# Kernel tuning notes

Measured on AMD Instinct MI355X. Metric: run time of the kernel, lower is better.

Reference implementation:

```python
import jax, jax.numpy as jnp
import numpy as np

D_MODEL, D_K, D_V, H, M = 1024, 64, 64, 16, 40


def setup_inputs() -> dict:
    key = jax.random.key(0)
    ks = jax.random.split(key, 16)
    b, nq, nk = 8, 1024, 1024
    inp = {
        "queries": jax.random.normal(ks[0], (b, nq, D_MODEL), jnp.float32),
        "keys": jax.random.normal(ks[1], (b, nk, D_MODEL), jnp.float32),
        "values": jax.random.normal(ks[2], (b, nk, D_MODEL), jnp.float32),
        "attention_mask": jax.random.randint(ks[3], (b, H, nq, nk), 0, 2) > 0,
        # Linear params, parametrized as x @ W + b (W has shape (in, out)).
        "Wq": jax.random.normal(ks[4], (D_MODEL, H * D_K), jnp.float32) * 0.03,
        "bq": jnp.zeros((H * D_K,), jnp.float32),
        "Wk": jax.random.normal(ks[5], (D_MODEL, H * D_K), jnp.float32) * 0.03,
        "bk": jnp.zeros((H * D_K,), jnp.float32),
        "Wv": jax.random.normal(ks[6], (D_MODEL, H * D_V), jnp.float32) * 0.03,
        "bv": jnp.zeros((H * D_V,), jnp.float32),
        "Wo": jax.random.normal(ks[7], (H * D_V, D_MODEL), jnp.float32) * 0.03,
        "bo": jnp.zeros((D_MODEL,), jnp.float32),
        # Memory slots: m_k ~ N(0, 1/d_k), m_v ~ N(0, 1/m), shape (1, m, h*d)
        "m_k": jax.random.normal(ks[8], (1, M, H * D_K), jnp.float32) / D_K,
        "m_v": jax.random.normal(ks[9], (1, M, H * D_V), jnp.float32) / M,
    }
    return inp


def reference(queries, keys, values, attention_mask, Wq, bq, Wk, bk, Wv, bv, Wo, bo, m_k, m_v):
    b, nq, _ = queries.shape
    nk = keys.shape[1]
    scale = jnp.asarray(np.sqrt(D_K), jnp.float32)

    # scaled memory slots, broadcast over batch
    mk = scale * jnp.broadcast_to(m_k, (b, M, H * D_K))
    mv = jnp.asarray(np.sqrt(M), jnp.float32) * jnp.broadcast_to(m_v, (b, M, H * D_V))

    q = (queries @ Wq + bq).reshape(b, nq, H, D_K).transpose(0, 2, 1, 3)       # b h nq dk
    k = jnp.concatenate([keys @ Wk + bk, mk], axis=1)                           # b (nk+m) h*dk
    k = k.reshape(b, nk + M, H, D_K).transpose(0, 2, 1, 3)                      # b h (nk+m) dk
    v = jnp.concatenate([values @ Wv + bv, mv], axis=1)
    v = v.reshape(b, nk + M, H, D_V).transpose(0, 2, 1, 3)                      # b h (nk+m) dv

    att = jnp.einsum('bhqd,bhkd->bhqk', q, k) / scale                           # b h nq (nk+m)
    # mask only real keys; memory slots always attendable
    att_real = jnp.where(attention_mask, -jnp.inf, att[:, :, :, :nk])
    att = jnp.concatenate([att_real, att[:, :, :, nk:]], axis=-1)
    att = jax.nn.softmax(att, axis=-1)

    out = jnp.einsum('bhqk,bhkd->bhqd', att, v)
    out = out.transpose(0, 2, 1, 3).reshape(b, nq, H * D_V)
    out = out @ Wo + bo
    return out, att
```

## Files before the change

kernel.cpp:

```cpp
#include <hip/hip_runtime.h>
#include <hip/hip_bf16.h>


#define B_ 8
#define NQ 1024
#define NK 1024
#define DM 1024
#define H_ 16
#define DK 64
#define NKM 1064
#define NKP 1104
#define PSTR 280

typedef __attribute__((ext_vector_type(8))) short bf16x8;
typedef __attribute__((ext_vector_type(4))) float f32x4;
typedef __attribute__((ext_vector_type(4))) short short4v;

static __device__ __forceinline__ short f2bf(float x) {
    __hip_bfloat16 h = __float2bfloat16(x);
    return __builtin_bit_cast(short, h);
}
static __device__ __forceinline__ float bf2f(short s) {
    unsigned int u = ((unsigned int)(unsigned short)s) << 16;
    return __builtin_bit_cast(float, u);
}

static __device__ __forceinline__ bf16x8 pack8(const float* __restrict__ p) {
    float4 f0 = *(const float4*)p;
    float4 f1 = *(const float4*)(p + 4);
    bf16x8 a;
    a[0] = f2bf(f0.x); a[1] = f2bf(f0.y); a[2] = f2bf(f0.z); a[3] = f2bf(f0.w);
    a[4] = f2bf(f1.x); a[5] = f2bf(f1.y); a[6] = f2bf(f1.z); a[7] = f2bf(f1.w);
    return a;
}

static __device__ __forceinline__ void gload16(const short* g, short* l) {
    __builtin_amdgcn_global_load_lds(
        (__attribute__((address_space(1))) void*)const_cast<short*>(g),
        (__attribute__((address_space(3))) void*)l, 16, 0, 0);
}

__global__ void detect_mask_kernel(const unsigned int* __restrict__ m, int n_dwords,
                                   int* __restrict__ flag) {
    __shared__ int any_big;
    if (threadIdx.x == 0) any_big = 0;
    __syncthreads();
    for (int i = threadIdx.x; i < n_dwords; i += blockDim.x)
        if (m[i] > 1u) any_big = 1;
    __syncthreads();
    if (threadIdx.x == 0) *flag = any_big ? 0 : 1;
}

__global__ void transpose_w_kernel(const float* __restrict__ W, short* __restrict__ WT) {
    __shared__ float t[32][33];
    int tx = threadIdx.x & 31, ty = threadIdx.x >> 5;
    int k0 = blockIdx.x * 32, n0 = blockIdx.y * 32;
#pragma unroll
    for (int r = 0; r < 4; r++)
        t[ty + 8 * r][tx] = W[(size_t)(k0 + ty + 8 * r) * DM + n0 + tx];
    __syncthreads();
#pragma unroll
    for (int r = 0; r < 4; r++)
        WT[(size_t)(n0 + ty + 8 * r) * DM + k0 + tx] = f2bf(t[tx][ty + 8 * r]);
}

__global__ void convert_bf16_kernel(const float* __restrict__ a, const float* __restrict__ b,
                                    const float* __restrict__ c, short* __restrict__ out) {
    const size_t NT = (size_t)B_ * NQ * DM;
    const size_t total = NT * 3;
    size_t i = ((size_t)blockIdx.x * 256 + threadIdx.x) * 8;
    const size_t step = (size_t)gridDim.x * 256 * 8;
    for (; i < total; i += step) {
        const float* src = (i < NT) ? (a + i) : (i < 2 * NT) ? (b + (i - NT)) : (c + (i - 2 * NT));
        *(bf16x8*)(out + i) = pack8(src);
    }
}

__global__ void fill_mem_kernel(const float* __restrict__ m_k, const float* __restrict__ m_v,
                                short* __restrict__ Kh, short* __restrict__ Vt) {
    int blk = blockIdx.x;
    int bh = blk / 20, rb = blk % 20;
    int r = rb * 4 + (threadIdx.x >> 6);
    int d = threadIdx.x & 63;
    int h = bh & 15;
    float kv = 0.f, vv = 0.f;
    if (r < 40) {
        kv = 8.0f * m_k[(size_t)(r * H_ + h) * DK + d];
        vv = 6.324555320336759f * m_v[(size_t)(r * H_ + h) * DK + d];
    }
    int kk = 1024 + r;
    Kh[((size_t)bh * NKP + kk) * 64 + d] = f2bf(kv);
    Vt[((size_t)bh * 64 + d) * NKP + kk] = f2bf(vv);
}

template <int MODE>
__global__ __launch_bounds__(256) void gemm_tile_kernel(
    const short* __restrict__ Ab, const short* __restrict__ BT,
    const float* __restrict__ bias,
    float* __restrict__ outF, short* __restrict__ outB) {
    __shared__ short As[2][4096];
    __shared__ short Bs[2][4096];

    const int tid = threadIdx.x;
    const int lane = tid & 63;
    const int wid = tid >> 6;
    int swz = (blockIdx.x & 7) * 64 + (blockIdx.x >> 3);
    const int mt = swz >> 3, nt = swz & 7;
    const int brow = mt * 128, bcol = nt * 128;
    const int wr = wid >> 1, wc = wid & 1;
    const int l15 = lane & 15, lg = lane >> 4;

    f32x4 acc[4][4];
#pragma unroll
    for (int m = 0; m < 4; m++)
#pragma unroll
        for (int n = 0; n < 4; n++) acc[m][n] = f32x4{0.f, 0.f, 0.f, 0.f};

    auto stage = [&](int buf, int k0) {
#pragma unroll
        for (int i = 0; i < 2; i++) {
            int c = tid + i * 256;
            int row = c >> 2, slot = c & 3;
            int base = (c & ~63) * 8;
            gload16(Ab + (size_t)(brow + row) * DM + k0 + slot * 8, &As[buf][base]);
            gload16(BT + (size_t)(bcol + row) * DM + k0 + slot * 8, &Bs[buf][base]);
        }
    };

    stage(0, 0);
    for (int kt = 0; kt < 32; ++kt) {
        __syncthreads();
        if (kt + 1 < 32) stage((kt + 1) & 1, (kt + 1) * 32);
        const short* Ab_ = As[kt & 1];
        const short* Bb_ = Bs[kt & 1];
        bf16x8 a[4], b[4];
#pragma unroll
        for (int m = 0; m < 4; m++)
            a[m] = *(const bf16x8*)(Ab_ + (wr * 64 + m * 16 + l15) * 32 + lg * 8);
#pragma unroll
        for (int n = 0; n < 4; n++)
            b[n] = *(const bf16x8*)(Bb_ + (wc * 64 + n * 16 + l15) * 32 + lg * 8);
#pragma unroll
        for (int m = 0; m < 4; m++)
#pragma unroll
            for (int n = 0; n < 4; n++)
                acc[m][n] = __builtin_amdgcn_mfma_f32_16x16x32_bf16(a[m], b[n], acc[m][n], 0, 0, 0);
    }

#pragma unroll
    for (int n = 0; n < 4; n++) {
        int col = bcol + wc * 64 + n * 16 + l15;
        float bval = bias[col];
#pragma unroll
        for (int m = 0; m < 4; m++) {
            int row0 = brow + wr * 64 + m * 16 + lg * 4;
            if (MODE == 3) {
#pragma unroll
                for (int r = 0; r < 4; r++)
                    outF[(size_t)(row0 + r) * DM + col] = acc[m][n][r] + bval;
            } else if (MODE == 0) {
                int h = col >> 6, d = col & 63;
#pragma unroll
                for (int r = 0; r < 4; r++) {
                    int row = row0 + r;
                    int b = row >> 10, q = row & 1023;
                    outB[((size_t)(b * H_ + h) * NQ + q) * 64 + d] = f2bf(acc[m][n][r] + bval);
                }
            } else if (MODE == 1) {
                int h = col >> 6, d = col & 63;
#pragma unroll
                for (int r = 0; r < 4; r++) {
                    int row = row0 + r;
                    int b = row >> 10, kk = row & 1023;
                    outB[((size_t)(b * H_ + h) * NKP + kk) * 64 + d] = f2bf(acc[m][n][r] + bval);
                }
            } else {
                int h = col >> 6, d = col & 63;
                int b = row0 >> 10, kk0 = row0 & 1023;
                short4v sv;
#pragma unroll
                for (int r = 0; r < 4; r++) sv[r] = f2bf(acc[m][n][r] + bval);
                *(short4v*)(outB + ((size_t)(b * H_ + h) * 64 + d) * NKP + kk0) = sv;
            }
        }
    }
}

__global__ __launch_bounds__(256) void attn_fused_kernel(
    const short* __restrict__ Qh, const short* __restrict__ Kh,
    const short* __restrict__ Vt,
    const unsigned char* __restrict__ mb, const int* __restrict__ mi,
    const int* __restrict__ flag,
    float* __restrict__ att, short* __restrict__ Ow) {
    __shared__ short Pl[4][16][PSTR];
    __shared__ float redS[4][16];

    int swz = (blockIdx.x & 7) * 1024 + (blockIdx.x >> 3);
    int bh = swz >> 6;
    int q0 = (swz & 63) * 16;
    int wid = threadIdx.x >> 6;
    int lane = threadIdx.x & 63;
    int l15 = lane & 15, lg = lane >> 4;

    const short* Qb = Qh + (size_t)bh * NQ * 64;
    const short* Kb = Kh + (size_t)bh * NKP * 64;
    const short* Vb = Vt + (size_t)bh * 64 * NKP;
    const int is32 = *flag;

    bf16x8 aq0 = *(const bf16x8*)(Qb + (size_t)(q0 + l15) * 64 + lg * 8);
    bf16x8 aq1 = *(const bf16x8*)(Qb + (size_t)(q0 + l15) * 64 + 32 + lg * 8);

    size_t qrow = (size_t)bh * NQ + q0 + l15;
    const int kkw = wid * 272;

    float rs = 0.f;
    for (int t = 0; t < 17; ++t) {
        int kt = kkw + t * 16;
        const short* Kr = Kb + (size_t)(kt + l15) * 64;
        bf16x8 k0 = *(const bf16x8*)(Kr + lg * 8);
        bf16x8 k1 = *(const bf16x8*)(Kr + 32 + lg * 8);
        f32x4 s = {0.f, 0.f, 0.f, 0.f};
        s = __builtin_amdgcn_mfma_f32_16x16x32_bf16(k0, aq0, s, 0, 0, 0);
        s = __builtin_amdgcn_mfma_f32_16x16x32_bf16(k1, aq1, s, 0, 0, 0);
        int kkbase = kt + lg * 4;
        unsigned mu = 0;
        if (kkbase < NK) {
            if (is32) {
                int4 mv = *(const int4*)(mi + qrow * NK + kkbase);
                mu = (mv.x ? 1u : 0u) | (mv.y ? 0x100u : 0u) |
                     (mv.z ? 0x10000u : 0u) | (mv.w ? 0x1000000u : 0u);
            } else {
                mu = *(const unsigned*)(mb + qrow * NK + kkbase);
            }
        }
        short4v pv;
#pragma unroll
        for (int r = 0; r < 4; r++) {
            bool dead = (kkbase + r >= NKM) || (((mu >> (8 * r)) & 0xffu) != 0u);
            float e = dead ? 0.f : __expf(s[r] * 0.125f);
            rs += e;
            pv[r] = f2bf(e);
        }
        *(short4v*)(&Pl[wid][l15][t * 16 + lg * 4]) = pv;
    }
    rs += __shfl_xor(rs, 16);
    rs += __shfl_xor(rs, 32);
    if (lg == 0) redS[wid][l15] = rs;
    __syncthreads();
    float invq = 1.f / (redS[0][l15] + redS[1][l15] + redS[2][l15] + redS[3][l15]);

    f32x4 po[4];
#pragma unroll
    for (int dt = 0; dt < 4; dt++) po[dt] = f32x4{0.f, 0.f, 0.f, 0.f};

    for (int pp = 0; pp < 9; ++pp) {
        int kks = kkw + pp * 32 + lg * 8;
        bool val = (pp < 8) | (lg < 2);
        bf16x8 a = bf16x8{0, 0, 0, 0, 0, 0, 0, 0};
        if (val) a = *(const bf16x8*)(&Pl[wid][l15][pp * 32 + lg * 8]);
        if (val && kks < NKM) {
            float4 w0, w1;
            w0.x = bf2f(a[0]) * invq; w0.y = bf2f(a[1]) * invq;
            w0.z = bf2f(a[2]) * invq; w0.w = bf2f(a[3]) * invq;
            w1.x = bf2f(a[4]) * invq; w1.y = bf2f(a[5]) * invq;
            w1.z = bf2f(a[6]) * invq; w1.w = bf2f(a[7]) * invq;
            *(float4*)(att + qrow * NKM + kks) = w0;
            *(float4*)(att + qrow * NKM + kks + 4) = w1;
        }
#pragma unroll
        for (int dt = 0; dt < 4; dt++) {
            bf16x8 bv = *(const bf16x8*)(Vb + (size_t)(dt * 16 + l15) * NKP + kkw + pp * 32 + lg * 8);
            po[dt] = __builtin_amdgcn_mfma_f32_16x16x32_bf16(a, bv, po[dt], 0, 0, 0);
        }
    }

    float* OredW = (float*)&Pl[wid][0][0];
#pragma unroll
    for (int dt = 0; dt < 4; dt++)
#pragma unroll
        for (int r = 0; r < 4; r++)
            OredW[(lg * 4 + r) * 68 + dt * 16 + l15] = po[dt][r];
    __syncthreads();

    int tq = threadIdx.x >> 4;
    int d0 = (threadIdx.x & 15) * 4;
    float4 o = {0.f, 0.f, 0.f, 0.f};
#pragma unroll
    for (int w = 0; w < 4; w++) {
        const float* Or = (const float*)&Pl[w][0][0];
        float4 v = *(const float4*)(&Or[tq * 68 + d0]);
        o.x += v.x; o.y += v.y; o.z += v.z; o.w += v.w;
    }
    float invt = 1.f / (redS[0][tq] + redS[1][tq] + redS[2][tq] + redS[3][tq]);
    int b = bh >> 4, h = bh & 15;
    short4v sv;
    sv[0] = f2bf(o.x * invt); sv[1] = f2bf(o.y * invt);
    sv[2] = f2bf(o.z * invt); sv[3] = f2bf(o.w * invt);
    *(short4v*)(Ow + ((size_t)b * NQ + q0 + tq) * DM + h * 64 + d0) = sv;
}

extern "C" void kernel_launch(void* const* d_in, const int* in_sizes, int n_in,
                              void* d_out, int out_size, void* d_ws, size_t ws_size,
                              hipStream_t stream) {
    const float* queries = (const float*)d_in[0];
    const float* keys    = (const float*)d_in[1];
    const float* values  = (const float*)d_in[2];
    const void*  mask    = d_in[3];
    const float* Wq = (const float*)d_in[4];
    const float* bq = (const float*)d_in[5];
    const float* Wk = (const float*)d_in[6];
    const float* bk = (const float*)d_in[7];
    const float* Wv = (const float*)d_in[8];
    const float* bv = (const float*)d_in[9];
    const float* Wo = (const float*)d_in[10];
    const float* bo = (const float*)d_in[11];
    const float* m_k = (const float*)d_in[12];
    const float* m_v = (const float*)d_in[13];

    short* WqT = (short*)d_ws;
    short* WkT = WqT + (size_t)DM * DM;
    short* WvT = WkT + (size_t)DM * DM;
    short* WoT = WvT + (size_t)DM * DM;
    short* Qh  = WoT + (size_t)DM * DM;
    short* Kh  = Qh + (size_t)B_ * H_ * NQ * DK;
    short* Vt  = Kh + (size_t)B_ * H_ * NKP * DK;
    short* Ow  = Vt + (size_t)B_ * H_ * DK * NKP;
    char*  after = (char*)(Ow + (size_t)B_ * NQ * DM);
    int*   flag = (int*)after;
    short* Qbf  = (short*)(after + 64);
    short* Kbf  = Qbf + (size_t)B_ * NQ * DM;
    short* Vbf  = Kbf + (size_t)B_ * NQ * DM;

    float* outO = (float*)d_out;
    float* att  = outO + (size_t)B_ * NQ * DM;

    detect_mask_kernel<<<1, 256, 0, stream>>>((const unsigned int*)mask, 4096, flag);

    dim3 tg(32, 32);
    transpose_w_kernel<<<tg, 256, 0, stream>>>(Wq, WqT);
    transpose_w_kernel<<<tg, 256, 0, stream>>>(Wk, WkT);
    transpose_w_kernel<<<tg, 256, 0, stream>>>(Wv, WvT);
    transpose_w_kernel<<<tg, 256, 0, stream>>>(Wo, WoT);

    convert_bf16_kernel<<<4096, 256, 0, stream>>>(queries, keys, values, Qbf);

    gemm_tile_kernel<0><<<512, 256, 0, stream>>>(Qbf, WqT, bq, nullptr, Qh);
    gemm_tile_kernel<1><<<512, 256, 0, stream>>>(Kbf, WkT, bk, nullptr, Kh);
    gemm_tile_kernel<2><<<512, 256, 0, stream>>>(Vbf, WvT, bv, nullptr, Vt);

    fill_mem_kernel<<<2560, 256, 0, stream>>>(m_k, m_v, Kh, Vt);

    attn_fused_kernel<<<8192, 256, 0, stream>>>(Qh, Kh, Vt,
                                                (const unsigned char*)mask, (const int*)mask,
                                                flag, att, Ow);

    gemm_tile_kernel<3><<<512, 256, 0, stream>>>(Ow, WoT, bo, outO, nullptr);
}
```

Measured before the change: 697.6 us.

## Fuse QK^T, exp, and PV MFMA into a single pass over key chunks

The attention kernel now computes scores for 32 keys per step using a permuted key-row mapping, so the exp'd probabilities land directly in the A-operand layout of the PV MFMA. The PV product therefore accumulates in the same loop instead of a second pass that reloads P from LDS. The second loop now only normalizes and writes the attention matrix. Launch bounds also request 4 blocks per CU, which may raise register pressure or cause spills.

```diff
diff --git a/kernel.cpp b/kernel.cpp
--- a/kernel.cpp
+++ b/kernel.cpp
@@ -186,7 +186,7 @@
     }
 }
 
-__global__ __launch_bounds__(256) void attn_fused_kernel(
+__global__ __launch_bounds__(256, 4) void attn_fused_kernel(
     const short* __restrict__ Qh, const short* __restrict__ Kh,
     const short* __restrict__ Vt,
     const unsigned char* __restrict__ mb, const int* __restrict__ mi,
@@ -212,65 +212,88 @@
 
     size_t qrow = (size_t)bh * NQ + q0 + l15;
     const int kkw = wid * 272;
-
+    const int rofs = ((l15 >> 2) << 3) + (l15 & 3);
+
+    f32x4 po[4];
+#pragma unroll
+    for (int dt = 0; dt < 4; dt++) po[dt] = f32x4{0.f, 0.f, 0.f, 0.f};
     float rs = 0.f;
-    for (int t = 0; t < 17; ++t) {
-        int kt = kkw + t * 16;
-        const short* Kr = Kb + (size_t)(kt + l15) * 64;
-        bf16x8 k0 = *(const bf16x8*)(Kr + lg * 8);
-        bf16x8 k1 = *(const bf16x8*)(Kr + 32 + lg * 8);
-        f32x4 s = {0.f, 0.f, 0.f, 0.f};
-        s = __builtin_amdgcn_mfma_f32_16x16x32_bf16(k0, aq0, s, 0, 0, 0);
-        s = __builtin_amdgcn_mfma_f32_16x16x32_bf16(k1, aq1, s, 0, 0, 0);
-        int kkbase = kt + lg * 4;
-        unsigned mu = 0;
-        if (kkbase < NK) {
+
+#pragma unroll 2
+    for (int pp = 0; pp < 9; ++pp) {
+        int ofs = pp * 32 + lg * 8;
+        int base = kkw + pp * 32;
+        int kkb = base + lg * 8;
+        const short* Kr0 = Kb + (size_t)(base + rofs) * 64;
+        bf16x8 k0a = *(const bf16x8*)(Kr0 + lg * 8);
+        bf16x8 k0b = *(const bf16x8*)(Kr0 + 32 + lg * 8);
+        bf16x8 k1a = *(const bf16x8*)(Kr0 + 256 + lg * 8);
+        bf16x8 k1b = *(const bf16x8*)(Kr0 + 256 + 32 + lg * 8);
+        bf16x8 bv0 = *(const bf16x8*)(Vb + (size_t)(l15) * NKP + kkb);
+        bf16x8 bv1 = *(const bf16x8*)(Vb + (size_t)(16 + l15) * NKP + kkb);
+        bf16x8 bv2 = *(const bf16x8*)(Vb + (size_t)(32 + l15) * NKP + kkb);
+        bf16x8 bv3 = *(const bf16x8*)(Vb + (size_t)(48 + l15) * NKP + kkb);
+        unsigned mlo = 0, mhi = 0;
+        if (kkb < NK) {
             if (is32) {
-                int4 mv = *(const int4*)(mi + qrow * NK + kkbase);
-                mu = (mv.x ? 1u : 0u) | (mv.y ? 0x100u : 0u) |
-                     (mv.z ? 0x10000u : 0u) | (mv.w ? 0x1000000u : 0u);
+                int4 ma = *(const int4*)(mi + qrow * NK + kkb);
+                int4 mc = *(const int4*)(mi + qrow * NK + kkb + 4);
+                mlo = (ma.x ? 1u : 0u) | (ma.y ? 0x100u : 0u) |
+                      (ma.z ? 0x10000u : 0u) | (ma.w ? 0x1000000u : 0u);
+                mhi = (mc.x ? 1u : 0u) | (mc.y ? 0x100u : 0u) |
+                      (mc.z ? 0x10000u : 0u) | (mc.w ? 0x1000000u : 0u);
             } else {
-                mu = *(const unsigned*)(mb + qrow * NK + kkbase);
+                uint2 mu = *(const uint2*)(mb + qrow * NK + kkb);
+                mlo = mu.x; mhi = mu.y;
             }
         }
-        short4v pv;
+        f32x4 s0 = {0.f, 0.f, 0.f, 0.f}, s1 = {0.f, 0.f, 0.f, 0.f};
+        s0 = __builtin_amdgcn_mfma_f32_16x16x32_bf16(k0a, aq0, s0, 0, 0, 0);
+        s0 = __builtin_amdgcn_mfma_f32_16x16x32_bf16(k0b, aq1, s0, 0, 0, 0);
+        s1 = __builtin_amdgcn_mfma_f32_16x16x32_bf16(k1a, aq0, s1, 0, 0, 0);
+        s1 = __builtin_amdgcn_mfma_f32_16x16x32_bf16(k1b, aq1, s1, 0, 0, 0);
+        bool live = (kkb < NKM) && (ofs < 272);
+        bf16x8 pa;
+        float e;
 #pragma unroll
         for (int r = 0; r < 4; r++) {
-            bool dead = (kkbase + r >= NKM) || (((mu >> (8 * r)) & 0xffu) != 0u);
-            float e = dead ? 0.f : __expf(s[r] * 0.125f);
+            e = (live && (((mlo >> (8 * r)) & 0xffu) == 0u)) ? __expf(s0[r] * 0.125f) : 0.f;
             rs += e;
-            pv[r] = f2bf(e);
-        }
-        *(short4v*)(&Pl[wid][l15][t * 16 + lg * 4]) = pv;
-    }
+            pa[r] = f2bf(e);
+        }
+#pragma unroll
+        for (int r = 0; r < 4; r++) {
+            e = (live && (((mhi >> (8 * r)) & 0xffu) == 0u)) ? __expf(s1[r] * 0.125f) : 0.f;
+            rs += e;
+            pa[4 + r] = f2bf(e);
+        }
+        po[0] = __builtin_amdgcn_mfma_f32_16x16x32_bf16(pa, bv0, po[0], 0, 0, 0);
+        po[1] = __builtin_amdgcn_mfma_f32_16x16x32_bf16(pa, bv1, po[1], 0, 0, 0);
+        po[2] = __builtin_amdgcn_mfma_f32_16x16x32_bf16(pa, bv2, po[2], 0, 0, 0);
+        po[3] = __builtin_amdgcn_mfma_f32_16x16x32_bf16(pa, bv3, po[3], 0, 0, 0);
+        if (ofs < 272)
+            *(bf16x8*)(&Pl[wid][l15][ofs]) = pa;
+    }
+
     rs += __shfl_xor(rs, 16);
     rs += __shfl_xor(rs, 32);
     if (lg == 0) redS[wid][l15] = rs;
     __syncthreads();
     float invq = 1.f / (redS[0][l15] + redS[1][l15] + redS[2][l15] + redS[3][l15]);
 
-    f32x4 po[4];
-#pragma unroll
-    for (int dt = 0; dt < 4; dt++) po[dt] = f32x4{0.f, 0.f, 0.f, 0.f};
-
+#pragma unroll 3
     for (int pp = 0; pp < 9; ++pp) {
-        int kks = kkw + pp * 32 + lg * 8;
-        bool val = (pp < 8) | (lg < 2);
-        bf16x8 a = bf16x8{0, 0, 0, 0, 0, 0, 0, 0};
-        if (val) a = *(const bf16x8*)(&Pl[wid][l15][pp * 32 + lg * 8]);
-        if (val && kks < NKM) {
+        int ofs = pp * 32 + lg * 8;
+        int kkb = kkw + ofs;
+        if (ofs < 272 && kkb < NKM) {
+            bf16x8 pa = *(const bf16x8*)(&Pl[wid][l15][ofs]);
             float4 w0, w1;
-            w0.x = bf2f(a[0]) * invq; w0.y = bf2f(a[1]) * invq;
-            w0.z = bf2f(a[2]) * invq; w0.w = bf2f(a[3]) * invq;
-            w1.x = bf2f(a[4]) * invq; w1.y = bf2f(a[5]) * invq;
-            w1.z = bf2f(a[6]) * invq; w1.w = bf2f(a[7]) * invq;
-            *(float4*)(att + qrow * NKM + kks) = w0;
-            *(float4*)(att + qrow * NKM + kks + 4) = w1;
-        }
-#pragma unroll
-        for (int dt = 0; dt < 4; dt++) {
-            bf16x8 bv = *(const bf16x8*)(Vb + (size_t)(dt * 16 + l15) * NKP + kkw + pp * 32 + lg * 8);
-            po[dt] = __builtin_amdgcn_mfma_f32_16x16x32_bf16(a, bv, po[dt], 0, 0, 0);
+            w0.x = bf2f(pa[0]) * invq; w0.y = bf2f(pa[1]) * invq;
+            w0.z = bf2f(pa[2]) * invq; w0.w = bf2f(pa[3]) * invq;
+            w1.x = bf2f(pa[4]) * invq; w1.y = bf2f(pa[5]) * invq;
+            w1.z = bf2f(pa[6]) * invq; w1.w = bf2f(pa[7]) * invq;
+            *(float4*)(att + qrow * NKM + kkb) = w0;
+            *(float4*)(att + qrow * NKM + kkb + 4) = w1;
         }
     }
 
```

Result: slower. 753.1 us (+8.0%).
